# Kernel tuning notes

Measured on AMD Instinct MI355X. Metric: run time of the kernel, lower is better.

## Reference

```python
import jax, jax.numpy as jnp
import numpy as np

H = 1024   # hidden_dim
F = 4096   # ffn_dim
E = 8      # n_experts
K = 2      # topk
B, S = 2, 1024


def setup_inputs() -> dict:
    key = jax.random.key(0)
    k0, k1, k2, k3, k4 = jax.random.split(key, 5)
    s = 0.02
    x = jax.random.normal(k0, (B, S, H), dtype=jnp.float32)
    Wr = jax.random.normal(k1, (E, H), dtype=jnp.float32) * s      # router Linear weight [E,H]
    W1 = jax.random.normal(k2, (E, H, F), dtype=jnp.float32) * s   # expert gate proj
    W3 = jax.random.normal(k3, (E, H, F), dtype=jnp.float32) * s   # expert up proj
    W2 = jax.random.normal(k4, (E, F, H), dtype=jnp.float32) * s   # expert down proj
    return {"x": x, "Wr": Wr, "W1": W1, "W2": W2, "W3": W3}


def reference(x, Wr, W1, W2, W3):
    b, s, h = x.shape
    xf = x.reshape(-1, h)                      # [T, H]
    T = xf.shape[0]
    # --- router ---
    logits = xf @ Wr.T                         # [T, E]
    probs = jax.nn.softmax(logits, axis=-1)
    _, idx = jax.lax.top_k(probs, K)           # [T, K] expert indices
    w = jnp.take_along_axis(probs, idx, axis=-1)
    w = w / w.sum(axis=-1, keepdims=True)      # renormalize selected weights
    # dense combine matrix [T, E]: zero for unselected experts
    combine = jnp.zeros((T, E), xf.dtype).at[jnp.arange(T)[:, None], idx].set(w)
    # --- experts (SwiGLU FFN, evaluated densely then masked by combine) ---
    gate = jax.nn.silu(jnp.einsum('th,ehf->tef', xf, W1))
    up = jnp.einsum('th,ehf->tef', xf, W3)
    hmid = gate * up                            # [T, E, F]
    out = jnp.einsum('te,tef,efh->th', combine, hmid, W2)
    return out.reshape(b, s, h)
```

## Files before the change

### kernel.cpp

```cpp
#include <hip/hip_runtime.h>
#include <hip/hip_bf16.h>
#include <math.h>

#define HD 1024
#define FD 4096
#define NE 8
#define NT 2048
#define BM 128
#define BN 128
#define BK 32

#define WS_LISTS   1024
#define WS_ROUTEW  (1024 + NE*NT*4)
#define WS_HMID    (1024 + NE*NT*4 + NT*2*4)

typedef __attribute__((ext_vector_type(8))) short bf16x8;
typedef __attribute__((ext_vector_type(4))) float f32x4;

static __device__ inline unsigned int pk_bf16(float a, float b) {
    __hip_bfloat162 h = __float22bfloat162_rn(make_float2(a, b));
    return *reinterpret_cast<unsigned int*>(&h);
}

__global__ void zero_out_kernel(float* __restrict__ out, int n, int* __restrict__ counts) {
    int i = blockIdx.x * blockDim.x + threadIdx.x;
    if (i < NE) counts[i] = 0;
    int stride = gridDim.x * blockDim.x;
    for (int j = i; j < n; j += stride) out[j] = 0.f;
}

__global__ __launch_bounds__(128)
void router_kernel(const float* __restrict__ x, const float* __restrict__ Wr,
                   int* __restrict__ counts, int* __restrict__ lists,
                   float* __restrict__ route_w) {
    int t = blockIdx.x;
    int tid = threadIdx.x;
    float acc[NE];
#pragma unroll
    for (int e = 0; e < NE; e++) acc[e] = 0.f;
    const float* xt = x + (size_t)t * HD;
    for (int h = tid; h < HD; h += 128) {
        float xv = xt[h];
#pragma unroll
        for (int e = 0; e < NE; e++) acc[e] += xv * Wr[e * HD + h];
    }
    __shared__ float red[NE][128];
#pragma unroll
    for (int e = 0; e < NE; e++) red[e][tid] = acc[e];
    __syncthreads();
    for (int s = 64; s > 0; s >>= 1) {
        if (tid < s) {
#pragma unroll
            for (int e = 0; e < NE; e++) red[e][tid] += red[e][tid + s];
        }
        __syncthreads();
    }
    if (tid == 0) {
        int i0 = 0; float l0 = red[0][0];
        for (int e = 1; e < NE; e++) { float v = red[e][0]; if (v > l0) { l0 = v; i0 = e; } }
        int i1 = -1; float l1 = -3.0e38f;
        for (int e = 0; e < NE; e++) {
            if (e == i0) continue;
            float v = red[e][0]; if (v > l1) { l1 = v; i1 = e; }
        }
        float w0 = 1.f / (1.f + expf(l1 - l0));
        float w1 = 1.f - w0;
        int s0 = atomicAdd(&counts[i0], 1);
        lists[i0 * NT + s0] = t * 2;
        route_w[t * 2] = w0;
        int s1 = atomicAdd(&counts[i1], 1);
        lists[i1 * NT + s1] = t * 2 + 1;
        route_w[t * 2 + 1] = w1;
    }
}

__global__ __launch_bounds__(256, 2)
void gemm1_kernel(const float* __restrict__ x, const float* __restrict__ W1,
                  const float* __restrict__ W3,
                  const int* __restrict__ counts, const int* __restrict__ lists,
                  unsigned short* __restrict__ hmid) {
    int e = blockIdx.z;
    int cnt = counts[e];
    int m0 = blockIdx.y * BM;
    if (m0 >= cnt) return;
    int n0 = blockIdx.x * BN;
    const float* W1e = W1 + (size_t)e * HD * FD;
    const float* W3e = W3 + (size_t)e * HD * FD;

    __shared__ __align__(16) unsigned short As[128 * 40];
    __shared__ __align__(16) unsigned short B1s[128 * 40];
    __shared__ __align__(16) unsigned short B3s[128 * 40];
    __shared__ int rp_s[128];
    __shared__ int rt_s[128];

    int tid = threadIdx.x;
    if (tid < 128) {
        int m = m0 + tid;
        int p = (m < cnt) ? lists[e * NT + m] : lists[e * NT];
        rp_s[tid] = p;
        rt_s[tid] = p >> 1;
    }
    __syncthreads();

    const int a_kq = tid & 7;
    const int a_mb = tid >> 3;
    const float* xr[4];
#pragma unroll
    for (int r = 0; r < 4; r++)
        xr[r] = x + (size_t)rt_s[a_mb + r * 32] * HD + a_kq * 4;

    const int b_n  = tid & 127;
    const int b_kh = tid >> 7;
    const float* b1p = W1e + (size_t)(b_kh * 16) * FD + n0 + b_n;
    const float* b3p = W3e + (size_t)(b_kh * 16) * FD + n0 + b_n;

    const int wv = tid >> 6;
    const int wr = wv >> 1, wc = wv & 1;
    const int lane = tid & 63;
    const int lm = lane & 15;
    const int lg = lane >> 4;

    f32x4 zf = {0.f, 0.f, 0.f, 0.f};
    f32x4 accG[4][4], accU[4][4];
#pragma unroll
    for (int i = 0; i < 4; i++)
#pragma unroll
        for (int j = 0; j < 4; j++) { accG[i][j] = zf; accU[i][j] = zf; }

    for (int h0 = 0; h0 < HD; h0 += BK) {
        float4 av[4];
#pragma unroll
        for (int r = 0; r < 4; r++) av[r] = *(const float4*)(xr[r] + h0);
        float b1v[16], b3v[16];
#pragma unroll
        for (int rr = 0; rr < 16; rr++) b1v[rr] = b1p[(size_t)(h0 + rr) * FD];
#pragma unroll
        for (int rr = 0; rr < 16; rr++) b3v[rr] = b3p[(size_t)(h0 + rr) * FD];

        __syncthreads();
#pragma unroll
        for (int r = 0; r < 4; r++) {
            uint2 w; w.x = pk_bf16(av[r].x, av[r].y); w.y = pk_bf16(av[r].z, av[r].w);
            *(uint2*)&As[(a_mb + r * 32) * 40 + a_kq * 4] = w;
        }
#pragma unroll
        for (int q = 0; q < 4; q++) {
            uint2 w; w.x = pk_bf16(b1v[q * 4 + 0], b1v[q * 4 + 1]);
            w.y = pk_bf16(b1v[q * 4 + 2], b1v[q * 4 + 3]);
            *(uint2*)&B1s[b_n * 40 + b_kh * 16 + q * 4] = w;
        }
#pragma unroll
        for (int q = 0; q < 4; q++) {
            uint2 w; w.x = pk_bf16(b3v[q * 4 + 0], b3v[q * 4 + 1]);
            w.y = pk_bf16(b3v[q * 4 + 2], b3v[q * 4 + 3]);
            *(uint2*)&B3s[b_n * 40 + b_kh * 16 + q * 4] = w;
        }
        __syncthreads();

        bf16x8 af[4], bf1[4], bf3[4];
#pragma unroll
        for (int i = 0; i < 4; i++)
            af[i] = *(const bf16x8*)&As[(wr * 64 + i * 16 + lm) * 40 + lg * 8];
#pragma unroll
        for (int j = 0; j < 4; j++) {
            bf1[j] = *(const bf16x8*)&B1s[(wc * 64 + j * 16 + lm) * 40 + lg * 8];
            bf3[j] = *(const bf16x8*)&B3s[(wc * 64 + j * 16 + lm) * 40 + lg * 8];
        }
#pragma unroll
        for (int i = 0; i < 4; i++)
#pragma unroll
            for (int j = 0; j < 4; j++) {
                accG[i][j] = __builtin_amdgcn_mfma_f32_16x16x32_bf16(af[i], bf1[j], accG[i][j], 0, 0, 0);
                accU[i][j] = __builtin_amdgcn_mfma_f32_16x16x32_bf16(af[i], bf3[j], accU[i][j], 0, 0, 0);
            }
    }

#pragma unroll
    for (int i = 0; i < 4; i++) {
#pragma unroll
        for (int r = 0; r < 4; r++) {
            int ml = wr * 64 + i * 16 + lg * 4 + r;
            int m = m0 + ml;
            if (m < cnt) {
                int p = rp_s[ml];
                unsigned short* hrow = hmid + (size_t)p * FD + n0 + wc * 64 + lm;
#pragma unroll
                for (int j = 0; j < 4; j++) {
                    float g = accG[i][j][r];
                    float u = accU[i][j][r];
                    float v = (g / (1.f + expf(-g))) * u;
                    __hip_bfloat16 hb = __float2bfloat16(v);
                    hrow[j * 16] = *reinterpret_cast<unsigned short*>(&hb);
                }
            }
        }
    }
}

__global__ __launch_bounds__(256, 2)
void gemm2_kernel(const unsigned short* __restrict__ hmid, const float* __restrict__ W2,
                  const int* __restrict__ counts, const int* __restrict__ lists,
                  const float* __restrict__ route_w, float* __restrict__ out) {
    int e = blockIdx.z & 7;
    int ks = blockIdx.z >> 3;
    int cnt = counts[e];
    int m0 = blockIdx.y * BM;
    if (m0 >= cnt) return;
    int n0 = blockIdx.x * BN;
    const float* W2e = W2 + (size_t)e * FD * HD;

    __shared__ __align__(16) unsigned short As[128 * 40];
    __shared__ __align__(16) unsigned short Bs[128 * 40];
    __shared__ int rp_s[128];
    __shared__ float rw_s[128];

    int tid = threadIdx.x;
    if (tid < 128) {
        int m = m0 + tid;
        int p = (m < cnt) ? lists[e * NT + m] : lists[e * NT];
        rp_s[tid] = p;
        rw_s[tid] = route_w[p];
    }
    __syncthreads();

    const int a_c = tid & 3;
    const int a_mb = tid >> 2;
    const unsigned short* ar[2];
#pragma unroll
    for (int r = 0; r < 2; r++)
        ar[r] = hmid + (size_t)rp_s[a_mb + r * 64] * FD + a_c * 8;

    const int b_n  = tid & 127;
    const int b_kh = tid >> 7;
    const float* bp = W2e + (size_t)(b_kh * 16) * HD + n0 + b_n;

    const int wv = tid >> 6;
    const int wr = wv >> 1, wc = wv & 1;
    const int lane = tid & 63;
    const int lm = lane & 15;
    const int lg = lane >> 4;

    f32x4 zf = {0.f, 0.f, 0.f, 0.f};
    f32x4 acc[4][4];
#pragma unroll
    for (int i = 0; i < 4; i++)
#pragma unroll
        for (int j = 0; j < 4; j++) acc[i][j] = zf;

    const int f_begin = ks * (FD / 2);
    const int f_end   = f_begin + FD / 2;
    for (int f0 = f_begin; f0 < f_end; f0 += BK) {
        uint4 avv[2];
#pragma unroll
        for (int r = 0; r < 2; r++) avv[r] = *(const uint4*)(ar[r] + f0);
        float bv[16];
#pragma unroll
        for (int rr = 0; rr < 16; rr++) bv[rr] = bp[(size_t)(f0 + rr) * HD];

        __syncthreads();
#pragma unroll
        for (int r = 0; r < 2; r++)
            *(uint4*)&As[(a_mb + r * 64) * 40 + a_c * 8] = avv[r];
#pragma unroll
        for (int q = 0; q < 4; q++) {
            uint2 w; w.x = pk_bf16(bv[q * 4 + 0], bv[q * 4 + 1]);
            w.y = pk_bf16(bv[q * 4 + 2], bv[q * 4 + 3]);
            *(uint2*)&Bs[b_n * 40 + b_kh * 16 + q * 4] = w;
        }
        __syncthreads();

        bf16x8 af[4], bf[4];
#pragma unroll
        for (int i = 0; i < 4; i++)
            af[i] = *(const bf16x8*)&As[(wr * 64 + i * 16 + lm) * 40 + lg * 8];
#pragma unroll
        for (int j = 0; j < 4; j++)
            bf[j] = *(const bf16x8*)&Bs[(wc * 64 + j * 16 + lm) * 40 + lg * 8];
#pragma unroll
        for (int i = 0; i < 4; i++)
#pragma unroll
            for (int j = 0; j < 4; j++)
                acc[i][j] = __builtin_amdgcn_mfma_f32_16x16x32_bf16(af[i], bf[j], acc[i][j], 0, 0, 0);
    }

#pragma unroll
    for (int i = 0; i < 4; i++) {
#pragma unroll
        for (int r = 0; r < 4; r++) {
            int ml = wr * 64 + i * 16 + lg * 4 + r;
            int m = m0 + ml;
            if (m < cnt) {
                int p = rp_s[ml];
                float w = rw_s[ml];
                int tok = p >> 1;
                float* orow = out + (size_t)tok * HD + n0 + wc * 64 + lm;
#pragma unroll
                for (int j = 0; j < 4; j++)
                    atomicAdd(&orow[j * 16], acc[i][j][r] * w);
            }
        }
    }
}

extern "C" void kernel_launch(void* const* d_in, const int* in_sizes, int n_in,
                              void* d_out, int out_size, void* d_ws, size_t ws_size,
                              hipStream_t stream) {
    const float* x  = (const float*)d_in[0];
    const float* Wr = (const float*)d_in[1];
    const float* W1 = (const float*)d_in[2];
    const float* W2 = (const float*)d_in[3];
    const float* W3 = (const float*)d_in[4];
    float* out = (float*)d_out;

    char* ws = (char*)d_ws;
    int*   counts  = (int*)(ws);
    int*   lists   = (int*)(ws + WS_LISTS);
    float* route_w = (float*)(ws + WS_ROUTEW);
    unsigned short* hmid = (unsigned short*)(ws + WS_HMID);

    hipLaunchKernelGGL(zero_out_kernel, dim3(2048), dim3(256), 0, stream,
                       out, NT * HD, counts);
    hipLaunchKernelGGL(router_kernel, dim3(NT), dim3(128), 0, stream,
                       x, Wr, counts, lists, route_w);
    hipLaunchKernelGGL(gemm1_kernel, dim3(FD / BN, NT / BM, NE), dim3(256), 0, stream,
                       x, W1, W3, counts, lists, hmid);
    hipLaunchKernelGGL(gemm2_kernel, dim3(HD / BN, NT / BM, NE * 2), dim3(256), 0, stream,
                       hmid, W2, counts, lists, route_w, out);
}
```

Measured before the change: 731.6 us.

## Pre-transpose weights to bf16, use global_load_lds, replace atomics with combine pass

Adds a prep kernel that converts x to bf16 and a transpose kernel that rewrites W1/W3 and W2 into K-contiguous bf16 buffers each call. The GEMMs then stage tiles with direct global-to-LDS 16-byte loads instead of strided fp32 loads plus in-register conversion. Block indices are remapped so tiles are spread across XCDs. The atomic scatter into out is replaced by writing per-pair, per-K-split partials and a separate combine kernel that applies the routing weights. The cost is an extra full pass over all expert weights per call, extra workspace traffic, and the loss of the LDS padding, which may cause bank conflicts.

```diff
diff --git a/kernel.cpp b/kernel.cpp
--- a/kernel.cpp
+++ b/kernel.cpp
@@ -12,21 +12,32 @@
 
 #define WS_LISTS   1024
 #define WS_ROUTEW  (1024 + NE*NT*4)
-#define WS_HMID    (1024 + NE*NT*4 + NT*2*4)
+#define WS_XB      ((size_t)1 << 20)
+#define WS_HMID    ((size_t)8 << 20)
+#define WS_WBUF    ((size_t)48 << 20)
+#define WS_OPAIR   ((size_t)112 << 20)
 
 typedef __attribute__((ext_vector_type(8))) short bf16x8;
 typedef __attribute__((ext_vector_type(4))) float f32x4;
 
-static __device__ inline unsigned int pk_bf16(float a, float b) {
+static __device__ __forceinline__ unsigned int pk_bf16(float a, float b) {
     __hip_bfloat162 h = __float22bfloat162_rn(make_float2(a, b));
     return *reinterpret_cast<unsigned int*>(&h);
 }
 
-__global__ void zero_out_kernel(float* __restrict__ out, int n, int* __restrict__ counts) {
-    int i = blockIdx.x * blockDim.x + threadIdx.x;
-    if (i < NE) counts[i] = 0;
-    int stride = gridDim.x * blockDim.x;
-    for (int j = i; j < n; j += stride) out[j] = 0.f;
+static __device__ __forceinline__ void gll16(const void* g, void* l) {
+    __builtin_amdgcn_global_load_lds(
+        (const __attribute__((address_space(1))) unsigned int*)g,
+        (__attribute__((address_space(3))) unsigned int*)l,
+        16, 0, 0);
+}
+
+__global__ void prep_kernel(const float* __restrict__ x, unsigned short* __restrict__ xb,
+                            int* __restrict__ counts) {
+    int idx = blockIdx.x * 256 + threadIdx.x;
+    if (idx < NE) counts[idx] = 0;
+    float4 v = *(const float4*)(x + (size_t)idx * 4);
+    *(uint2*)(xb + (size_t)idx * 4) = make_uint2(pk_bf16(v.x, v.y), pk_bf16(v.z, v.w));
 }
 
 __global__ __launch_bounds__(128)
@@ -74,51 +85,83 @@
     }
 }
 
+__global__ __launch_bounds__(256)
+void transp_kernel(const float* __restrict__ srcA, const float* __restrict__ srcB,
+                   unsigned short* __restrict__ dst, int R, int C) {
+    __shared__ float tile[64][65];
+    int z = blockIdx.z;
+    const float* src = (z < 8) ? (srcA + (size_t)z * R * C) : (srcB + (size_t)(z - 8) * R * C);
+    unsigned short* d = dst + (size_t)z * R * C;
+    int c0 = blockIdx.x * 64, r0 = blockIdx.y * 64;
+    int t = threadIdx.x;
+    int rr = t >> 4, cc = (t & 15) * 4;
+#pragma unroll
+    for (int i = 0; i < 4; i++) {
+        int r = rr + i * 16;
+        float4 v = *(const float4*)(src + (size_t)(r0 + r) * C + c0 + cc);
+        tile[cc + 0][r] = v.x; tile[cc + 1][r] = v.y;
+        tile[cc + 2][r] = v.z; tile[cc + 3][r] = v.w;
+    }
+    __syncthreads();
+    int cl = t >> 2, rc = (t & 3) * 16;
+    unsigned int o[8];
+#pragma unroll
+    for (int i = 0; i < 8; i++)
+        o[i] = pk_bf16(tile[cl][rc + 2 * i], tile[cl][rc + 2 * i + 1]);
+    unsigned short* dp = d + (size_t)(c0 + cl) * R + r0 + rc;
+    *(uint4*)(dp)     = make_uint4(o[0], o[1], o[2], o[3]);
+    *(uint4*)(dp + 8) = make_uint4(o[4], o[5], o[6], o[7]);
+}
+
 __global__ __launch_bounds__(256, 2)
-void gemm1_kernel(const float* __restrict__ x, const float* __restrict__ W1,
-                  const float* __restrict__ W3,
+void gemm1_kernel(const unsigned short* __restrict__ xb, const unsigned short* __restrict__ wbuf,
                   const int* __restrict__ counts, const int* __restrict__ lists,
                   unsigned short* __restrict__ hmid) {
-    int e = blockIdx.z;
+    int xcd = blockIdx.x;
+    int y = blockIdx.y;
+    int en = xcd + 8 * (y >> 4);
+    int mblk = y & 15;
+    int e = en >> 5;
+    int nblk = en & 31;
     int cnt = counts[e];
-    int m0 = blockIdx.y * BM;
+    int m0 = mblk * BM;
     if (m0 >= cnt) return;
-    int n0 = blockIdx.x * BN;
-    const float* W1e = W1 + (size_t)e * HD * FD;
-    const float* W3e = W3 + (size_t)e * HD * FD;
-
-    __shared__ __align__(16) unsigned short As[128 * 40];
-    __shared__ __align__(16) unsigned short B1s[128 * 40];
-    __shared__ __align__(16) unsigned short B3s[128 * 40];
+    int n0 = nblk * BN;
+    const unsigned short* W1b = wbuf + (size_t)e * FD * HD;
+    const unsigned short* W3b = wbuf + (size_t)(8 + e) * FD * HD;
+
+    __shared__ __align__(16) unsigned short As[128 * 32];
+    __shared__ __align__(16) unsigned short B1s[128 * 32];
+    __shared__ __align__(16) unsigned short B3s[128 * 32];
     __shared__ int rp_s[128];
-    __shared__ int rt_s[128];
 
     int tid = threadIdx.x;
     if (tid < 128) {
         int m = m0 + tid;
-        int p = (m < cnt) ? lists[e * NT + m] : lists[e * NT];
-        rp_s[tid] = p;
-        rt_s[tid] = p >> 1;
+        rp_s[tid] = (m < cnt) ? lists[e * NT + m] : lists[e * NT];
     }
     __syncthreads();
 
-    const int a_kq = tid & 7;
-    const int a_mb = tid >> 3;
-    const float* xr[4];
-#pragma unroll
-    for (int r = 0; r < 4; r++)
-        xr[r] = x + (size_t)rt_s[a_mb + r * 32] * HD + a_kq * 4;
-
-    const int b_n  = tid & 127;
-    const int b_kh = tid >> 7;
-    const float* b1p = W1e + (size_t)(b_kh * 16) * FD + n0 + b_n;
-    const float* b3p = W3e + (size_t)(b_kh * 16) * FD + n0 + b_n;
-
-    const int wv = tid >> 6;
-    const int wr = wv >> 1, wc = wv & 1;
+    const int w = tid >> 6;
     const int lane = tid & 63;
-    const int lm = lane & 15;
-    const int lg = lane >> 4;
+    const int srow = lane >> 2;
+    const int schunk = lane & 3;
+
+    const unsigned short *gA[2], *gB1[2], *gB3[2];
+    unsigned short *lA[2], *lB1[2], *lB3[2];
+#pragma unroll
+    for (int q = 0; q < 2; q++) {
+        int row = w * 32 + q * 16 + srow;
+        gA[q]  = xb  + (size_t)(rp_s[row] >> 1) * HD + schunk * 8;
+        gB1[q] = W1b + (size_t)(n0 + row) * HD + schunk * 8;
+        gB3[q] = W3b + (size_t)(n0 + row) * HD + schunk * 8;
+        lA[q]  = &As [(w * 32 + q * 16) * 32];
+        lB1[q] = &B1s[(w * 32 + q * 16) * 32];
+        lB3[q] = &B3s[(w * 32 + q * 16) * 32];
+    }
+
+    const int wr = w >> 1, wc = w & 1;
+    const int lm = lane & 15, lg = lane >> 4;
 
     f32x4 zf = {0.f, 0.f, 0.f, 0.f};
     f32x4 accG[4][4], accU[4][4];
@@ -128,50 +171,30 @@
         for (int j = 0; j < 4; j++) { accG[i][j] = zf; accU[i][j] = zf; }
 
     for (int h0 = 0; h0 < HD; h0 += BK) {
-        float4 av[4];
-#pragma unroll
-        for (int r = 0; r < 4; r++) av[r] = *(const float4*)(xr[r] + h0);
-        float b1v[16], b3v[16];
-#pragma unroll
-        for (int rr = 0; rr < 16; rr++) b1v[rr] = b1p[(size_t)(h0 + rr) * FD];
-#pragma unroll
-        for (int rr = 0; rr < 16; rr++) b3v[rr] = b3p[(size_t)(h0 + rr) * FD];
-
-        __syncthreads();
-#pragma unroll
-        for (int r = 0; r < 4; r++) {
-            uint2 w; w.x = pk_bf16(av[r].x, av[r].y); w.y = pk_bf16(av[r].z, av[r].w);
-            *(uint2*)&As[(a_mb + r * 32) * 40 + a_kq * 4] = w;
-        }
-#pragma unroll
-        for (int q = 0; q < 4; q++) {
-            uint2 w; w.x = pk_bf16(b1v[q * 4 + 0], b1v[q * 4 + 1]);
-            w.y = pk_bf16(b1v[q * 4 + 2], b1v[q * 4 + 3]);
-            *(uint2*)&B1s[b_n * 40 + b_kh * 16 + q * 4] = w;
-        }
-#pragma unroll
-        for (int q = 0; q < 4; q++) {
-            uint2 w; w.x = pk_bf16(b3v[q * 4 + 0], b3v[q * 4 + 1]);
-            w.y = pk_bf16(b3v[q * 4 + 2], b3v[q * 4 + 3]);
-            *(uint2*)&B3s[b_n * 40 + b_kh * 16 + q * 4] = w;
-        }
-        __syncthreads();
-
-        bf16x8 af[4], bf1[4], bf3[4];
+        __syncthreads();
+#pragma unroll
+        for (int q = 0; q < 2; q++) {
+            gll16(gA[q] + h0, lA[q]);
+            gll16(gB1[q] + h0, lB1[q]);
+            gll16(gB3[q] + h0, lB3[q]);
+        }
+        __syncthreads();
+
+        bf16x8 af[4], b1f[4], b3f[4];
 #pragma unroll
         for (int i = 0; i < 4; i++)
-            af[i] = *(const bf16x8*)&As[(wr * 64 + i * 16 + lm) * 40 + lg * 8];
+            af[i] = *(const bf16x8*)&As[(wr * 64 + i * 16 + lm) * 32 + lg * 8];
 #pragma unroll
         for (int j = 0; j < 4; j++) {
-            bf1[j] = *(const bf16x8*)&B1s[(wc * 64 + j * 16 + lm) * 40 + lg * 8];
-            bf3[j] = *(const bf16x8*)&B3s[(wc * 64 + j * 16 + lm) * 40 + lg * 8];
+            b1f[j] = *(const bf16x8*)&B1s[(wc * 64 + j * 16 + lm) * 32 + lg * 8];
+            b3f[j] = *(const bf16x8*)&B3s[(wc * 64 + j * 16 + lm) * 32 + lg * 8];
         }
 #pragma unroll
         for (int i = 0; i < 4; i++)
 #pragma unroll
             for (int j = 0; j < 4; j++) {
-                accG[i][j] = __builtin_amdgcn_mfma_f32_16x16x32_bf16(af[i], bf1[j], accG[i][j], 0, 0, 0);
-                accU[i][j] = __builtin_amdgcn_mfma_f32_16x16x32_bf16(af[i], bf3[j], accU[i][j], 0, 0, 0);
+                accG[i][j] = __builtin_amdgcn_mfma_f32_16x16x32_bf16(af[i], b1f[j], accG[i][j], 0, 0, 0);
+                accU[i][j] = __builtin_amdgcn_mfma_f32_16x16x32_bf16(af[i], b3f[j], accU[i][j], 0, 0, 0);
             }
     }
 
@@ -198,47 +221,52 @@
 }
 
 __global__ __launch_bounds__(256, 2)
-void gemm2_kernel(const unsigned short* __restrict__ hmid, const float* __restrict__ W2,
+void gemm2_kernel(const unsigned short* __restrict__ hmid, const unsigned short* __restrict__ wbuf,
                   const int* __restrict__ counts, const int* __restrict__ lists,
-                  const float* __restrict__ route_w, float* __restrict__ out) {
-    int e = blockIdx.z & 7;
-    int ks = blockIdx.z >> 3;
+                  float* __restrict__ opair) {
+    int xcd = blockIdx.x;
+    int y = blockIdx.y;
+    int grp = xcd + 8 * (y >> 4);
+    int mblk = y & 15;
+    int ks = grp >> 6;
+    int rest = grp & 63;
+    int e = rest >> 3;
+    int nblk = rest & 7;
     int cnt = counts[e];
-    int m0 = blockIdx.y * BM;
+    int m0 = mblk * BM;
     if (m0 >= cnt) return;
-    int n0 = blockIdx.x * BN;
-    const float* W2e = W2 + (size_t)e * FD * HD;
-
-    __shared__ __align__(16) unsigned short As[128 * 40];
-    __shared__ __align__(16) unsigned short Bs[128 * 40];
+    int n0 = nblk * BN;
+    const unsigned short* W2b = wbuf + (size_t)e * HD * FD;
+
+    __shared__ __align__(16) unsigned short As[128 * 32];
+    __shared__ __align__(16) unsigned short Bs[128 * 32];
     __shared__ int rp_s[128];
-    __shared__ float rw_s[128];
 
     int tid = threadIdx.x;
     if (tid < 128) {
         int m = m0 + tid;
-        int p = (m < cnt) ? lists[e * NT + m] : lists[e * NT];
-        rp_s[tid] = p;
-        rw_s[tid] = route_w[p];
+        rp_s[tid] = (m < cnt) ? lists[e * NT + m] : lists[e * NT];
     }
     __syncthreads();
 
-    const int a_c = tid & 3;
-    const int a_mb = tid >> 2;
-    const unsigned short* ar[2];
-#pragma unroll
-    for (int r = 0; r < 2; r++)
-        ar[r] = hmid + (size_t)rp_s[a_mb + r * 64] * FD + a_c * 8;
-
-    const int b_n  = tid & 127;
-    const int b_kh = tid >> 7;
-    const float* bp = W2e + (size_t)(b_kh * 16) * HD + n0 + b_n;
-
-    const int wv = tid >> 6;
-    const int wr = wv >> 1, wc = wv & 1;
+    const int w = tid >> 6;
     const int lane = tid & 63;
-    const int lm = lane & 15;
-    const int lg = lane >> 4;
+    const int srow = lane >> 2;
+    const int schunk = lane & 3;
+
+    const unsigned short *gA[2], *gB[2];
+    unsigned short *lA[2], *lB[2];
+#pragma unroll
+    for (int q = 0; q < 2; q++) {
+        int row = w * 32 + q * 16 + srow;
+        gA[q] = hmid + (size_t)rp_s[row] * FD + schunk * 8;
+        gB[q] = W2b + (size_t)(n0 + row) * FD + schunk * 8;
+        lA[q] = &As[(w * 32 + q * 16) * 32];
+        lB[q] = &Bs[(w * 32 + q * 16) * 32];
+    }
+
+    const int wr = w >> 1, wc = w & 1;
+    const int lm = lane & 15, lg = lane >> 4;
 
     f32x4 zf = {0.f, 0.f, 0.f, 0.f};
     f32x4 acc[4][4];
@@ -248,34 +276,23 @@
         for (int j = 0; j < 4; j++) acc[i][j] = zf;
 
     const int f_begin = ks * (FD / 2);
-    const int f_end   = f_begin + FD / 2;
+    const int f_end = f_begin + FD / 2;
     for (int f0 = f_begin; f0 < f_end; f0 += BK) {
-        uint4 avv[2];
-#pragma unroll
-        for (int r = 0; r < 2; r++) avv[r] = *(const uint4*)(ar[r] + f0);
-        float bv[16];
-#pragma unroll
-        for (int rr = 0; rr < 16; rr++) bv[rr] = bp[(size_t)(f0 + rr) * HD];
-
-        __syncthreads();
-#pragma unroll
-        for (int r = 0; r < 2; r++)
-            *(uint4*)&As[(a_mb + r * 64) * 40 + a_c * 8] = avv[r];
-#pragma unroll
-        for (int q = 0; q < 4; q++) {
-            uint2 w; w.x = pk_bf16(bv[q * 4 + 0], bv[q * 4 + 1]);
-            w.y = pk_bf16(bv[q * 4 + 2], bv[q * 4 + 3]);
-            *(uint2*)&Bs[b_n * 40 + b_kh * 16 + q * 4] = w;
+        __syncthreads();
+#pragma unroll
+        for (int q = 0; q < 2; q++) {
+            gll16(gA[q] + f0, lA[q]);
+            gll16(gB[q] + f0, lB[q]);
         }
         __syncthreads();
 
         bf16x8 af[4], bf[4];
 #pragma unroll
         for (int i = 0; i < 4; i++)
-            af[i] = *(const bf16x8*)&As[(wr * 64 + i * 16 + lm) * 40 + lg * 8];
+            af[i] = *(const bf16x8*)&As[(wr * 64 + i * 16 + lm) * 32 + lg * 8];
 #pragma unroll
         for (int j = 0; j < 4; j++)
-            bf[j] = *(const bf16x8*)&Bs[(wc * 64 + j * 16 + lm) * 40 + lg * 8];
+            bf[j] = *(const bf16x8*)&Bs[(wc * 64 + j * 16 + lm) * 32 + lg * 8];
 #pragma unroll
         for (int i = 0; i < 4; i++)
 #pragma unroll
@@ -291,15 +308,35 @@
             int m = m0 + ml;
             if (m < cnt) {
                 int p = rp_s[ml];
-                float w = rw_s[ml];
-                int tok = p >> 1;
-                float* orow = out + (size_t)tok * HD + n0 + wc * 64 + lm;
-#pragma unroll
-                for (int j = 0; j < 4; j++)
-                    atomicAdd(&orow[j * 16], acc[i][j][r] * w);
+                float* op = opair + ((size_t)ks * (2 * NT) + p) * HD + n0 + wc * 64 + lm;
+#pragma unroll
+                for (int j = 0; j < 4; j++) op[j * 16] = acc[i][j][r];
             }
         }
     }
+}
+
+__global__ __launch_bounds__(256)
+void combine_kernel(const float* __restrict__ opair, const float* __restrict__ route_w,
+                    float* __restrict__ out) {
+    int idx = blockIdx.x * 256 + threadIdx.x;
+    int tok = idx >> 8;
+    int hc = (idx & 255) * 4;
+    const float* o0 = opair;
+    const float* o1 = opair + (size_t)(2 * NT) * HD;
+    size_t r0 = (size_t)(2 * tok) * HD + hc;
+    size_t r1 = (size_t)(2 * tok + 1) * HD + hc;
+    float w0 = route_w[2 * tok], w1 = route_w[2 * tok + 1];
+    float4 a = *(const float4*)(o0 + r0);
+    float4 b = *(const float4*)(o1 + r0);
+    float4 c = *(const float4*)(o0 + r1);
+    float4 d = *(const float4*)(o1 + r1);
+    float4 r;
+    r.x = w0 * (a.x + b.x) + w1 * (c.x + d.x);
+    r.y = w0 * (a.y + b.y) + w1 * (c.y + d.y);
+    r.z = w0 * (a.z + b.z) + w1 * (c.z + d.z);
+    r.w = w0 * (a.w + b.w) + w1 * (c.w + d.w);
+    *(float4*)(out + (size_t)tok * HD + hc) = r;
 }
 
 extern "C" void kernel_launch(void* const* d_in, const int* in_sizes, int n_in,
@@ -316,14 +353,22 @@
     int*   counts  = (int*)(ws);
     int*   lists   = (int*)(ws + WS_LISTS);
     float* route_w = (float*)(ws + WS_ROUTEW);
+    unsigned short* xb   = (unsigned short*)(ws + WS_XB);
     unsigned short* hmid = (unsigned short*)(ws + WS_HMID);
-
-    hipLaunchKernelGGL(zero_out_kernel, dim3(2048), dim3(256), 0, stream,
-                       out, NT * HD, counts);
+    unsigned short* wbuf = (unsigned short*)(ws + WS_WBUF);
+    float* opair = (float*)(ws + WS_OPAIR);
+
+    hipLaunchKernelGGL(prep_kernel, dim3(2048), dim3(256), 0, stream, x, xb, counts);
     hipLaunchKernelGGL(router_kernel, dim3(NT), dim3(128), 0, stream,
                        x, Wr, counts, lists, route_w);
-    hipLaunchKernelGGL(gemm1_kernel, dim3(FD / BN, NT / BM, NE), dim3(256), 0, stream,
-                       x, W1, W3, counts, lists, hmid);
-    hipLaunchKernelGGL(gemm2_kernel, dim3(HD / BN, NT / BM, NE * 2), dim3(256), 0, stream,
-                       hmid, W2, counts, lists, route_w, out);
-}
+    hipLaunchKernelGGL(transp_kernel, dim3(FD / 64, HD / 64, 16), dim3(256), 0, stream,
+                       W1, W3, wbuf, HD, FD);
+    hipLaunchKernelGGL(gemm1_kernel, dim3(8, 512), dim3(256), 0, stream,
+                       xb, wbuf, counts, lists, hmid);
+    hipLaunchKernelGGL(transp_kernel, dim3(HD / 64, FD / 64, 8), dim3(256), 0, stream,
+                       W2, W2, wbuf, FD, HD);
+    hipLaunchKernelGGL(gemm2_kernel, dim3(8, 256), dim3(256), 0, stream,
+                       hmid, wbuf, counts, lists, opair);
+    hipLaunchKernelGGL(combine_kernel, dim3(2048), dim3(256), 0, stream,
+                       opair, route_w, out);
+}
```

Result: faster. 666.6 us (-8.9%).
